# Performance work log

Hardware: AMD Instinct MI355X
Metric: run time of the kernel (lower is better)

The kernel has to match this reference:

```python
import jax, jax.numpy as jnp
import numpy as np

# Module hyperparameters (from init_kwargs)
N_S = 128                      # n_scalars
L2_IDX = (0, 1, 2, 3, 4, 5, 6) # l2_indices
N_L2 = len(L2_IDX) + 1         # selected l=2 kernels + their sum -> 8
H = 256                        # hidden multiplicity
B = 2048                       # batch
K = 8                          # number of kernels in kernel_t2s


def _w3j_222():
    """Real-basis Wigner 3j for (2e,2e)->2e, Frobenius norm 1 (e3nn convention).
    Built as tr(Qa Qb Qc) over an orthonormal basis of symmetric traceless 3x3
    matrices (the unique invariant 3-tensor on the 5-dim l=2 irrep)."""
    Q = np.zeros((5, 3, 3))
    s = 1.0 / np.sqrt(2.0)
    Q[0, 0, 1] = Q[0, 1, 0] = s
    Q[1, 1, 2] = Q[1, 2, 1] = s
    Q[2] = np.diag([-1.0, -1.0, 2.0]) / np.sqrt(6.0)
    Q[3, 0, 2] = Q[3, 2, 0] = s
    Q[4, 0, 0] = s
    Q[4, 1, 1] = -s
    C = np.einsum('aij,bjk,cki->abc', Q, Q, Q)
    return C / np.linalg.norm(C)

C222 = jnp.asarray(_w3j_222(), dtype=jnp.float32)

# e3nn FullyConnectedTensorProduct path normalization ('component'/'element'):
# coeff = sqrt((2*l_out+1) / sum over paths into same output of mul1*mul2)
C0 = float(np.sqrt(1.0 / (N_S**2 + N_L2**2)))            # paths into Hx0e: 0x0->0, 2x2->0
C2 = float(np.sqrt(5.0 / (2 * N_S * N_L2 + N_L2**2)))    # paths into Hx2e: 0x2, 2x0, 2x2
C2B = float(np.sqrt(5.0 / (3 * H**2)))                   # tp2 paths into 1x2e
INV_S5 = float(1.0 / np.sqrt(5.0))                       # w3j(l,l,0) = I/sqrt(2l+1), l=2


def setup_inputs() -> dict:
    key = jax.random.key(0)
    ks = jax.random.split(key, 10)
    f32 = jnp.float32
    return {
        'scalars': jax.random.normal(ks[0], (B, N_S), f32),
        'kernel_t2s': jax.random.normal(ks[1], (B, K, 5), f32),
        'W000': jax.random.normal(ks[2], (N_S, N_S, H), f32),
        'W220': jax.random.normal(ks[3], (N_L2, N_L2, H), f32),
        'W022': jax.random.normal(ks[4], (N_S, N_L2, H), f32),
        'W202': jax.random.normal(ks[5], (N_L2, N_S, H), f32),
        'W222': jax.random.normal(ks[6], (N_L2, N_L2, H), f32),
        'V022': jax.random.normal(ks[7], (H, H, 1), f32),
        'V202': jax.random.normal(ks[8], (H, H, 1), f32),
        'V222': jax.random.normal(ks[9], (H, H, 1), f32),
    }


def reference(scalars, kernel_t2s, W000, W220, W022, W202, W222, V022, V202, V222):
    ee = lambda *a: jnp.einsum(*a, optimize='optimal')
    idx = jnp.asarray(L2_IDX)
    # build tp input: [B, n_s] scalars  ++  [B, n_l2, 5] l=2 features
    t = jnp.concatenate([kernel_t2s[:, idx, :],
                         kernel_t2s.sum(axis=1, keepdims=True)], axis=1)  # [B, N_L2, 5]
    s = scalars                                                            # [B, N_S]

    # tp1(x, x): Hx0e + Hx2e
    y0 = C0 * (ee('uvw,zu,zv->zw', W000, s, s)
               + INV_S5 * ee('uvw,zui,zvi->zw', W220, t, t))               # [B, H]
    y2 = C2 * (INV_S5 * (ee('uvw,zu,zvk->zwk', W022, s, t)
                         + ee('uvw,zuk,zv->zwk', W202, t, s))
               + ee('uvw,ijk,zui,zvj->zwk', W222, C222, t, t))             # [B, H, 5]

    # tp2(y, y): 1x2e
    out = C2B * (INV_S5 * (ee('uvw,zu,zvk->zwk', V022, y0, y2)
                           + ee('uvw,zuk,zv->zwk', V202, y2, y0))
                 + ee('uvw,ijk,zui,zvj->zwk', V222, C222, y2, y2))         # [B, 1, 5]
    return out[:, 0, :]                                                    # [B, 5]
```

## Files before the change

kernel.cpp:

```cpp
#include <hip/hip_runtime.h>
#include <stdint.h>
#include <stddef.h>


#define NS     128
#define NL2    8
#define HH     256

#define KPAIR  8256
#define KPAD   8448
#define GLEN   64
#define KSPLIT 16
#define CHUNK  528
#define KT     16
#define NTILES 33

#define C0F  0.00779729f
#define C2F  0.04865619f
#define C2BF 0.005042948f
#define IS5  0.44721360f

constexpr size_t OFF_C222 = 0;
constexpr size_t OFF_PU   = 128;
constexpr size_t OFF_PV   = 8576;
constexpr size_t OFF_T    = 17024;
constexpr size_t OFF_GSYM = 98944;
constexpr size_t OFF_W1   = 230016;
constexpr size_t OFF_W222 = 754304;
constexpr size_t OFF_VBS  = 770688;
constexpr size_t OFF_VC   = 836224;
constexpr size_t OFF_Y0   = 901760;
constexpr size_t OFF_ACP  = 1426048;
constexpr size_t WS_FLOATS = 1950336;

#define SEG_T    81920
#define SEG_PUV  90368
#define SEG_W1   614656
#define SEG_W222 631040
#define SEG_VBS  696576
#define SEG_VC   762112
#define SEG_GS   893184
#define SEG_Y0   1417472

__global__ __launch_bounds__(256) void prep_k(
    const float* __restrict__ kt2s, const float* __restrict__ W022,
    const float* __restrict__ W202, const float* __restrict__ W222,
    const float* __restrict__ V022, const float* __restrict__ V202,
    const float* __restrict__ V222, float* __restrict__ ws) {
  const int tid = threadIdx.x;

  if (blockIdx.x == 0) {
    __shared__ float cv[125];
    __shared__ float inv;
    float val = 0.f;
    if (tid < 125) {
      float Q[45];
      #pragma unroll
      for (int q = 0; q < 45; ++q) Q[q] = 0.f;
      const float s2 = 0.70710678f, s6 = 0.40824829f;
      Q[0*9+0*3+1] = s2;  Q[0*9+1*3+0] = s2;
      Q[1*9+1*3+2] = s2;  Q[1*9+2*3+1] = s2;
      Q[2*9+0*3+0] = -s6; Q[2*9+1*3+1] = -s6; Q[2*9+2*3+2] = 2.f*s6;
      Q[3*9+0*3+2] = s2;  Q[3*9+2*3+0] = s2;
      Q[4*9+0*3+0] = s2;  Q[4*9+1*3+1] = -s2;
      const int a = tid/25, b = (tid/5)%5, c = tid%5;
      for (int i = 0; i < 3; ++i)
        for (int j = 0; j < 3; ++j)
          for (int k = 0; k < 3; ++k)
            val += Q[a*9+i*3+j]*Q[b*9+j*3+k]*Q[c*9+k*3+i];
      cv[tid] = val;
    }
    __syncthreads();
    if (tid == 0) {
      float sq = 0.f;
      for (int p = 0; p < 125; ++p) sq += cv[p]*cv[p];
      inv = 1.0f/sqrtf(sq);
    }
    __syncthreads();
    if (tid < 125) ws[OFF_C222 + tid] = val*inv;
    return;
  }

  int*   pu    = (int*)(ws + OFF_PU);
  int*   pv    = (int*)(ws + OFF_PV);
  const int stride = (gridDim.x - 1)*256;
  for (int i = (blockIdx.x - 1)*256 + tid; i < SEG_Y0; i += stride) {
    if (i < SEG_T) {
      int z = i/40, r = i - z*40, u = r/5, ii = r - u*5;
      float v;
      if (u < 7) v = kt2s[z*40 + u*5 + ii];
      else {
        v = 0.f;
        for (int k = 0; k < 8; ++k) v += kt2s[z*40 + k*5 + ii];
      }
      ws[OFF_T + i] = v;
    } else if (i < SEG_PUV) {
      int p = i - SEG_T;
      int u = 0, vv = 0;
      if (p < KPAIR) {
        int rem = p;
        while (rem >= NS - u) { rem -= NS - u; ++u; }
        vv = u + rem;
      } else if (p < KPAIR + 36) {
        int q = p - KPAIR;
        while (q >= NL2 - u) { q -= NL2 - u; ++u; }
        vv = u + q;
      }
      pu[p] = u; pv[p] = vv;
    } else if (i < SEG_W1) {
      int j = i - SEG_PUV;
      int u = j >> 12, col = j & 4095;
      float v;
      if (col < 2048) {
        int vv = col >> 8, w = col & 255;
        v = (C2F*IS5)*W022[(u*NL2 + vv)*HH + w];
      } else {
        int u2 = (col - 2048) >> 8, w = col & 255;
        v = (C2F*IS5)*W202[(u2*NS + u)*HH + w];
      }
      ws[OFF_W1 + j] = v;
    } else if (i < SEG_W222) {
      int j = i - SEG_W1;
      ws[OFF_W222 + j] = C2F*W222[j];
    } else if (i < SEG_VBS) {
      int j = i - SEG_W222;
      int u = j >> 8, c = j & 255;
      ws[OFF_VBS + j] = (C2BF*IS5)*(V022[u*HH + c] + V202[c*HH + u]);
    } else if (i < SEG_VC) {
      int j = i - SEG_VBS;
      ws[OFF_VC + j] = C2BF*V222[j];
    } else if (i < SEG_GS) {
      int j = i - SEG_VC;
      int z = j >> 6, q = j & 63;
      float v = 0.f;
      if (q < 36) {
        int qq = q, u = 0;
        while (qq >= NL2 - u) { qq -= NL2 - u; ++u; }
        int vv = u + qq;
        const float* kz = kt2s + (size_t)z*40;
        #pragma unroll
        for (int ii = 0; ii < 5; ++ii) {
          float tu, tv;
          if (u < 7) tu = kz[u*5 + ii];
          else { tu = 0.f; for (int k = 0; k < 8; ++k) tu += kz[k*5 + ii]; }
          if (vv < 7) tv = kz[vv*5 + ii];
          else { tv = 0.f; for (int k = 0; k < 8; ++k) tv += kz[k*5 + ii]; }
          v += tu*tv;
        }
      }
      ws[OFF_GSYM + j] = v;
    } else {
      ws[OFF_Y0 + (i - SEG_GS)] = 0.f;
    }
  }
}

__global__ __launch_bounds__(256) void gemm_y0_k(
    const float* __restrict__ s, const float* __restrict__ W000,
    const float* __restrict__ W220, float* __restrict__ ws) {
  const int* pu = (const int*)(ws + OFF_PU);
  const int* pv = (const int*)(ws + OFF_PV);
  const float* Gsym = ws + OFF_GSYM;
  float* y0 = ws + OFF_Y0;

  __shared__ float s_s[64][129];
  __shared__ __align__(16) float As[KT][64];
  __shared__ __align__(16) float Bs[KT][256];

  const int tid  = threadIdx.x;
  const int ks   = blockIdx.x & 15, mt = blockIdx.x >> 4;
  const int z0   = mt*64;
  const int kbase = ks*CHUNK;
  const int lane = tid & 63, wave = tid >> 6;
  const int tx   = tid & 31, ty   = tid >> 5;

  for (int e = 0; e < 8; ++e) {
    int f4 = e*256 + tid;
    int row = f4 >> 5, c4 = f4 & 31;
    float4 v = reinterpret_cast<const float4*>(s + (size_t)(z0 + row)*NS)[c4];
    s_s[row][c4*4+0] = v.x; s_s[row][c4*4+1] = v.y;
    s_s[row][c4*4+2] = v.z; s_s[row][c4*4+3] = v.w;
  }

  float acc[8][8];
  #pragma unroll
  for (int i = 0; i < 8; ++i)
    #pragma unroll
    for (int j = 0; j < 8; ++j) acc[i][j] = 0.f;

  for (int tt = 0; tt < NTILES; ++tt) {
    const int k0 = kbase + tt*KT;
    __syncthreads();
    #pragma unroll
    for (int e = 0; e < 4; ++e) {
      int row = e*4 + wave;
      int p = k0 + row;
      float4 val;
      if (p < KPAIR) {
        int u = pu[p], v = pv[p];
        float4 a = *reinterpret_cast<const float4*>(&W000[((size_t)(u*NS + v))*HH + lane*4]);
        if (u != v) {
          float4 b = *reinterpret_cast<const float4*>(&W000[((size_t)(v*NS + u))*HH + lane*4]);
          val = make_float4(C0F*(a.x+b.x), C0F*(a.y+b.y), C0F*(a.z+b.z), C0F*(a.w+b.w));
        } else {
          val = make_float4(C0F*a.x, C0F*a.y, C0F*a.z, C0F*a.w);
        }
      } else if (p < KPAIR + 36) {
        int u = pu[p], v = pv[p];
        const float sc = C0F*IS5;
        float4 a = *reinterpret_cast<const float4*>(&W220[(u*NL2 + v)*HH + lane*4]);
        if (u != v) {
          float4 b = *reinterpret_cast<const float4*>(&W220[(v*NL2 + u)*HH + lane*4]);
          val = make_float4(sc*(a.x+b.x), sc*(a.y+b.y), sc*(a.z+b.z), sc*(a.w+b.w));
        } else {
          val = make_float4(sc*a.x, sc*a.y, sc*a.z, sc*a.w);
        }
      } else {
        val = make_float4(0.f, 0.f, 0.f, 0.f);
      }
      *reinterpret_cast<float4*>(&Bs[row][lane*4]) = val;
    }
    #pragma unroll
    for (int e = 0; e < 4; ++e) {
      int kk = e*4 + wave;
      int k = k0 + kk;
      float a;
      if (k < KPAIR) a = s_s[lane][pu[k]]*s_s[lane][pv[k]];
      else {
        int q = k - KPAIR;
        a = (q < GLEN) ? Gsym[(size_t)(z0 + lane)*GLEN + q] : 0.f;
      }
      As[kk][lane] = a;
    }
    __syncthreads();
    #pragma unroll
    for (int kk = 0; kk < KT; ++kk) {
      float4 a0 = *reinterpret_cast<const float4*>(&As[kk][ty*8]);
      float4 a1 = *reinterpret_cast<const float4*>(&As[kk][ty*8+4]);
      float4 b0 = *reinterpret_cast<const float4*>(&Bs[kk][tx*4]);
      float4 b1 = *reinterpret_cast<const float4*>(&Bs[kk][128 + tx*4]);
      float am[8] = {a0.x,a0.y,a0.z,a0.w,a1.x,a1.y,a1.z,a1.w};
      float bn[8] = {b0.x,b0.y,b0.z,b0.w,b1.x,b1.y,b1.z,b1.w};
      #pragma unroll
      for (int mi = 0; mi < 8; ++mi)
        #pragma unroll
        for (int ni = 0; ni < 8; ++ni)
          acc[mi][ni] += am[mi]*bn[ni];
    }
  }
  #pragma unroll
  for (int mi = 0; mi < 8; ++mi) {
    int z = z0 + ty*8 + mi;
    #pragma unroll
    for (int ni = 0; ni < 8; ++ni) {
      int col = (ni < 4) ? (tx*4 + ni) : (128 + tx*4 + (ni-4));
      atomicAdd(&y0[(size_t)z*HH + col], acc[mi][ni]);
    }
  }
}

__global__ __launch_bounds__(256) void gemm_rm_k(
    const float* __restrict__ A, const float* __restrict__ B,
    float* __restrict__ C, int M, int N, int K) {
  __shared__ __align__(16) float As[32][68];
  __shared__ __align__(16) float Bs[32][68];
  const int tid = threadIdx.x, tx = tid & 15, ty = tid >> 4;
  const int n0 = blockIdx.x*64, m0 = blockIdx.y*64;
  float acc[4][4];
  #pragma unroll
  for (int i = 0; i < 4; ++i)
    #pragma unroll
    for (int j = 0; j < 4; ++j) acc[i][j] = 0.f;

  for (int k0 = 0; k0 < K; k0 += 32) {
    __syncthreads();
    #pragma unroll
    for (int e = 0; e < 2; ++e) {
      int r = e*32 + (tid >> 3);
      int kc = (tid & 7)*4;
      float4 v = *reinterpret_cast<const float4*>(&A[(size_t)(m0+r)*K + k0 + kc]);
      As[kc+0][r] = v.x; As[kc+1][r] = v.y; As[kc+2][r] = v.z; As[kc+3][r] = v.w;
    }
    #pragma unroll
    for (int e = 0; e < 2; ++e) {
      int idx = e*256 + tid;
      int r = idx >> 4, c4 = idx & 15;
      float4 v = *reinterpret_cast<const float4*>(&B[(size_t)(k0+r)*N + n0 + c4*4]);
      *reinterpret_cast<float4*>(&Bs[r][c4*4]) = v;
    }
    __syncthreads();
    #pragma unroll
    for (int kk = 0; kk < 32; ++kk) {
      float4 av = *reinterpret_cast<const float4*>(&As[kk][ty*4]);
      float4 bv = *reinterpret_cast<const float4*>(&Bs[kk][tx*4]);
      float am[4] = {av.x, av.y, av.z, av.w};
      float bn[4] = {bv.x, bv.y, bv.z, bv.w};
      #pragma unroll
      for (int i = 0; i < 4; ++i)
        #pragma unroll
        for (int j = 0; j < 4; ++j) acc[i][j] += am[i]*bn[j];
    }
  }
  #pragma unroll
  for (int i = 0; i < 4; ++i) {
    float4 v = make_float4(acc[i][0], acc[i][1], acc[i][2], acc[i][3]);
    *reinterpret_cast<float4*>(&C[(size_t)(m0 + ty*4 + i)*N + n0 + tx*4]) = v;
  }
}

__global__ __launch_bounds__(256) void mega_k(
    const float* __restrict__ scalars, const float* __restrict__ ws,
    float* __restrict__ out) {
  const float* tg    = ws + OFF_T;
  const float* W1    = ws + OFF_W1;
  const float* W222c = ws + OFF_W222;
  const float* VC    = ws + OFF_VC;
  const float* acp   = ws + OFF_ACP;
  const float* c222g = ws + OFF_C222;

  __shared__ float ts[8][40];
  __shared__ float c2s[125];
  __shared__ __align__(16) float sb[8][128];
  __shared__ __align__(16) float ovl[10240];
  float* tC  = ovl;
  float* RsF = ovl + 1600;
  float* y2s = ovl;

  const int tid = threadIdx.x;
  const int zg0 = blockIdx.x*8;
  const int lane = tid & 63, wv = tid >> 6;

  if (tid < 125) c2s[tid] = c222g[tid];
  for (int r = tid; r < 320; r += 256) {
    int z = r/40, c = r - z*40;
    ts[z][c] = tg[(size_t)(zg0 + z)*40 + c];
  }
  {
    int z = tid >> 5, c4 = tid & 31;
    float4 v = reinterpret_cast<const float4*>(scalars + (size_t)(zg0 + z)*NS)[c4];
    sb[z][c4*4+0] = v.x; sb[z][c4*4+1] = v.y;
    sb[z][c4*4+2] = v.z; sb[z][c4*4+3] = v.w;
  }
  __syncthreads();

  for (int idx = tid; idx < 1600; idx += 256) {
    int z = idx/200, r = idx - z*200, v = r/25, ik = r - v*25;
    int i = ik/5, k = ik - i*5;
    float a = 0.f;
    #pragma unroll
    for (int j = 0; j < 5; ++j) a += c2s[(i*5+j)*5 + k]*ts[z][v*5+j];
    tC[idx] = a;
  }
  __syncthreads();
  for (int idx = tid; idx < 2560; idx += 256) {
    int uv = idx/40, r = idx - uv*40, z = r/5, k = r - z*5;
    int u = uv >> 3, v = uv & 7;
    float a = 0.f;
    #pragma unroll
    for (int ii = 0; ii < 5; ++ii) a += ts[z][u*5+ii]*tC[z*200 + v*25 + ii*5 + k];
    RsF[idx] = a;
  }
  __syncthreads();

  float acc[8][5];
  #pragma unroll
  for (int z = 0; z < 8; ++z)
    #pragma unroll
    for (int k = 0; k < 5; ++k) acc[z][k] = 0.f;

  for (int vg = 0; vg < 4; ++vg) {
    float av[4][8];
    #pragma unroll
    for (int vi = 0; vi < 4; ++vi)
      #pragma unroll
      for (int z = 0; z < 8; ++z) av[vi][z] = 0.f;
    for (int u4 = 0; u4 < 128; u4 += 4) {
      float4 szv[8];
      #pragma unroll
      for (int z = 0; z < 8; ++z) szv[z] = *reinterpret_cast<const float4*>(&sb[z][u4]);
      #pragma unroll
      for (int uu = 0; uu < 4; ++uu) {
        #pragma unroll
        for (int vi = 0; vi < 4; ++vi) {
          float w1v = W1[(size_t)(u4+uu)*4096 + (vg*4+vi)*256 + tid];
          #pragma unroll
          for (int z = 0; z < 8; ++z) {
            float su = (uu==0)?szv[z].x:(uu==1)?szv[z].y:(uu==2)?szv[z].z:szv[z].w;
            av[vi][z] += su*w1v;
          }
        }
      }
    }
    #pragma unroll
    for (int vi = 0; vi < 4; ++vi) {
      int vmap = (vg*4 + vi) & 7;
      #pragma unroll
      for (int z = 0; z < 8; ++z)
        #pragma unroll
        for (int k = 0; k < 5; ++k)
          acc[z][k] += av[vi][z]*ts[z][vmap*5+k];
    }
  }

  for (int uv = 0; uv < 64; ++uv) {
    float wvv = W222c[uv*256 + tid];
    #pragma unroll
    for (int c4 = 0; c4 < 10; ++c4) {
      float4 rv = *reinterpret_cast<const float4*>(&RsF[uv*40 + c4*4]);
      acc[(c4*4+0)/5][(c4*4+0)%5] += wvv*rv.x;
      acc[(c4*4+1)/5][(c4*4+1)%5] += wvv*rv.y;
      acc[(c4*4+2)/5][(c4*4+2)%5] += wvv*rv.z;
      acc[(c4*4+3)/5][(c4*4+3)%5] += wvv*rv.w;
    }
  }

  __syncthreads();
  #pragma unroll
  for (int z = 0; z < 8; ++z)
    #pragma unroll
    for (int k = 0; k < 5; ++k)
      y2s[z*1280 + k*256 + tid] = acc[z][k];
  __syncthreads();

  float hacc[2][5][4];
  #pragma unroll
  for (int zz = 0; zz < 2; ++zz)
    #pragma unroll
    for (int i = 0; i < 5; ++i)
      #pragma unroll
      for (int j = 0; j < 4; ++j) hacc[zz][i][j] = 0.f;

  for (int u4 = 0; u4 < 256; u4 += 4) {
    float vc[4][4];
    #pragma unroll
    for (int uu = 0; uu < 4; ++uu)
      #pragma unroll
      for (int j = 0; j < 4; ++j)
        vc[uu][j] = VC[(size_t)(u4+uu)*256 + lane + 64*j];
    #pragma unroll
    for (int zz = 0; zz < 2; ++zz) {
      int z = wv*2 + zz;
      #pragma unroll
      for (int i = 0; i < 5; ++i) {
        float4 yv = *reinterpret_cast<const float4*>(&y2s[z*1280 + i*256 + u4]);
        float ya[4] = {yv.x, yv.y, yv.z, yv.w};
        #pragma unroll
        for (int uu = 0; uu < 4; ++uu)
          #pragma unroll
          for (int j = 0; j < 4; ++j)
            hacc[zz][i][j] += ya[uu]*vc[uu][j];
      }
    }
  }

  float outp[2][5];
  #pragma unroll
  for (int zz = 0; zz < 2; ++zz)
    #pragma unroll
    for (int k = 0; k < 5; ++k) outp[zz][k] = 0.f;

  for (int j = 0; j < 4; ++j) {
    int v = lane + 64*j;
    #pragma unroll
    for (int zz = 0; zz < 2; ++zz) {
      int z = wv*2 + zz;
      float y2v[5];
      #pragma unroll
      for (int jp = 0; jp < 5; ++jp) y2v[jp] = y2s[z*1280 + jp*256 + v];
      float avv = acp[(size_t)(zg0 + z)*256 + v];
      #pragma unroll
      for (int k = 0; k < 5; ++k) outp[zz][k] += avv*y2v[k];
      #pragma unroll
      for (int i = 0; i < 5; ++i) {
        float hv = hacc[zz][i][j];
        #pragma unroll
        for (int jp = 0; jp < 5; ++jp) {
          float pj = hv*y2v[jp];
          #pragma unroll
          for (int k = 0; k < 5; ++k)
            outp[zz][k] += pj*c2s[i*25 + jp*5 + k];
        }
      }
    }
  }

  #pragma unroll
  for (int zz = 0; zz < 2; ++zz)
    #pragma unroll
    for (int k = 0; k < 5; ++k) {
      float vsum = outp[zz][k];
      #pragma unroll
      for (int off = 32; off > 0; off >>= 1) vsum += __shfl_xor(vsum, off, 64);
      if (lane == 0) out[(size_t)(zg0 + wv*2 + zz)*5 + k] = vsum;
    }
}

extern "C" void kernel_launch(void* const* d_in, const int* in_sizes, int n_in,
                              void* d_out, int out_size, void* d_ws, size_t ws_size,
                              hipStream_t stream) {
  (void)in_sizes; (void)n_in; (void)out_size;
  const float* scalars = (const float*)d_in[0];
  const float* kt2s    = (const float*)d_in[1];
  const float* W000    = (const float*)d_in[2];
  const float* W220    = (const float*)d_in[3];
  const float* W022    = (const float*)d_in[4];
  const float* W202    = (const float*)d_in[5];
  const float* W222    = (const float*)d_in[6];
  const float* V022    = (const float*)d_in[7];
  const float* V202    = (const float*)d_in[8];
  const float* V222    = (const float*)d_in[9];
  float* out = (float*)d_out;
  float* ws  = (float*)d_ws;
  if (ws_size < WS_FLOATS*sizeof(float)) return;

  prep_k<<<1025, 256, 0, stream>>>(kt2s, W022, W202, W222, V022, V202, V222, ws);
  gemm_y0_k<<<512, 256, 0, stream>>>(scalars, W000, W220, ws);
  gemm_rm_k<<<dim3(4, 32), 256, 0, stream>>>(ws + OFF_Y0, ws + OFF_VBS,
                                             (float*)(ws + OFF_ACP), 2048, 256, 256);
  mega_k<<<256, 256, 0, stream>>>(scalars, ws, out);
}
```

Baseline: 585.0 us.

## Double-buffer y0 GEMM, split N tiles, transpose scalars, drop W1 repack

The y0 pair-GEMM now splits the 256 output columns into two 128-wide tiles, doubling the grid and halving accumulators per thread. It double-buffers the A/B shared tiles with register prefetch so the next tile's loads overlap the current tile's math. The A operand is read from column-major (transposed) copies of the scalars and the Gram matrix built in prep instead of a per-block shared scalar tile. The W022/W202 repack into W1 is removed, and mega_k reads the raw weights and applies the scale itself, which cuts prep work and workspace at the cost of strided weight loads and redundant B-tile loads across the two N halves.

```diff
diff --git a/kernel.cpp b/kernel.cpp
--- a/kernel.cpp
+++ b/kernel.cpp
@@ -6,6 +6,7 @@
 #define NS     128
 #define NL2    8
 #define HH     256
+#define NB     2048
 
 #define KPAIR  8256
 #define KPAD   8448
@@ -24,27 +25,27 @@
 constexpr size_t OFF_PU   = 128;
 constexpr size_t OFF_PV   = 8576;
 constexpr size_t OFF_T    = 17024;
-constexpr size_t OFF_GSYM = 98944;
-constexpr size_t OFF_W1   = 230016;
-constexpr size_t OFF_W222 = 754304;
-constexpr size_t OFF_VBS  = 770688;
-constexpr size_t OFF_VC   = 836224;
-constexpr size_t OFF_Y0   = 901760;
-constexpr size_t OFF_ACP  = 1426048;
-constexpr size_t WS_FLOATS = 1950336;
+constexpr size_t OFF_W222 = 98944;
+constexpr size_t OFF_VBS  = 115328;
+constexpr size_t OFF_VC   = 180864;
+constexpr size_t OFF_ST   = 246400;
+constexpr size_t OFF_GT   = 508544;
+constexpr size_t OFF_Y0   = 639616;
+constexpr size_t OFF_ACP  = 1163904;
+constexpr size_t WS_FLOATS = 1688192;
 
 #define SEG_T    81920
 #define SEG_PUV  90368
-#define SEG_W1   614656
-#define SEG_W222 631040
-#define SEG_VBS  696576
-#define SEG_VC   762112
-#define SEG_GS   893184
-#define SEG_Y0   1417472
+#define SEG_W222 106752
+#define SEG_VBS  172288
+#define SEG_VC   237824
+#define SEG_ST   499968
+#define SEG_GT   631040
+#define SEG_END  1155328
 
 __global__ __launch_bounds__(256) void prep_k(
-    const float* __restrict__ kt2s, const float* __restrict__ W022,
-    const float* __restrict__ W202, const float* __restrict__ W222,
+    const float* __restrict__ scalars, const float* __restrict__ kt2s,
+    const float* __restrict__ W222,
     const float* __restrict__ V022, const float* __restrict__ V202,
     const float* __restrict__ V222, float* __restrict__ ws) {
   const int tid = threadIdx.x;
@@ -81,10 +82,10 @@
     return;
   }
 
-  int*   pu    = (int*)(ws + OFF_PU);
-  int*   pv    = (int*)(ws + OFF_PV);
+  int* pu = (int*)(ws + OFF_PU);
+  int* pv = (int*)(ws + OFF_PV);
   const int stride = (gridDim.x - 1)*256;
-  for (int i = (blockIdx.x - 1)*256 + tid; i < SEG_Y0; i += stride) {
+  for (int i = (blockIdx.x - 1)*256 + tid; i < SEG_END; i += stride) {
     if (i < SEG_T) {
       int z = i/40, r = i - z*40, u = r/5, ii = r - u*5;
       float v;
@@ -107,20 +108,8 @@
         vv = u + q;
       }
       pu[p] = u; pv[p] = vv;
-    } else if (i < SEG_W1) {
+    } else if (i < SEG_W222) {
       int j = i - SEG_PUV;
-      int u = j >> 12, col = j & 4095;
-      float v;
-      if (col < 2048) {
-        int vv = col >> 8, w = col & 255;
-        v = (C2F*IS5)*W022[(u*NL2 + vv)*HH + w];
-      } else {
-        int u2 = (col - 2048) >> 8, w = col & 255;
-        v = (C2F*IS5)*W202[(u2*NS + u)*HH + w];
-      }
-      ws[OFF_W1 + j] = v;
-    } else if (i < SEG_W222) {
-      int j = i - SEG_W1;
       ws[OFF_W222 + j] = C2F*W222[j];
     } else if (i < SEG_VBS) {
       int j = i - SEG_W222;
@@ -129,9 +118,13 @@
     } else if (i < SEG_VC) {
       int j = i - SEG_VBS;
       ws[OFF_VC + j] = C2BF*V222[j];
-    } else if (i < SEG_GS) {
+    } else if (i < SEG_ST) {
       int j = i - SEG_VC;
-      int z = j >> 6, q = j & 63;
+      int u = j >> 11, z = j & 2047;
+      ws[OFF_ST + j] = scalars[(size_t)z*NS + u];
+    } else if (i < SEG_GT) {
+      int j = i - SEG_ST;
+      int q = j >> 11, z = j & 2047;
       float v = 0.f;
       if (q < 36) {
         int qq = q, u = 0;
@@ -148,114 +141,135 @@
           v += tu*tv;
         }
       }
-      ws[OFF_GSYM + j] = v;
+      ws[OFF_GT + j] = v;
     } else {
-      ws[OFF_Y0 + (i - SEG_GS)] = 0.f;
+      ws[OFF_Y0 + (i - SEG_GT)] = 0.f;
     }
   }
 }
 
-__global__ __launch_bounds__(256) void gemm_y0_k(
-    const float* __restrict__ s, const float* __restrict__ W000,
-    const float* __restrict__ W220, float* __restrict__ ws) {
+__global__ __launch_bounds__(256, 4) void gemm_y0_k(
+    const float* __restrict__ W000, const float* __restrict__ W220,
+    float* __restrict__ ws) {
   const int* pu = (const int*)(ws + OFF_PU);
   const int* pv = (const int*)(ws + OFF_PV);
-  const float* Gsym = ws + OFF_GSYM;
+  const float* sT = ws + OFF_ST;
+  const float* gT = ws + OFF_GT;
   float* y0 = ws + OFF_Y0;
 
-  __shared__ float s_s[64][129];
-  __shared__ __align__(16) float As[KT][64];
-  __shared__ __align__(16) float Bs[KT][256];
-
-  const int tid  = threadIdx.x;
-  const int ks   = blockIdx.x & 15, mt = blockIdx.x >> 4;
-  const int z0   = mt*64;
+  __shared__ __align__(16) float As[2][KT][64];
+  __shared__ __align__(16) float Bs[2][KT][128];
+
+  const int tid = threadIdx.x;
+  const int bid = blockIdx.x;
+  const int ks = bid & 15, mtnt = bid >> 4;
+  const int mt = mtnt >> 1, nt = mtnt & 1;
+  const int z0 = mt*64, n0 = nt*128;
   const int kbase = ks*CHUNK;
-  const int lane = tid & 63, wave = tid >> 6;
-  const int tx   = tid & 31, ty   = tid >> 5;
-
-  for (int e = 0; e < 8; ++e) {
-    int f4 = e*256 + tid;
-    int row = f4 >> 5, c4 = f4 & 31;
-    float4 v = reinterpret_cast<const float4*>(s + (size_t)(z0 + row)*NS)[c4];
-    s_s[row][c4*4+0] = v.x; s_s[row][c4*4+1] = v.y;
-    s_s[row][c4*4+2] = v.z; s_s[row][c4*4+3] = v.w;
-  }
-
-  float acc[8][8];
-  #pragma unroll
-  for (int i = 0; i < 8; ++i)
-    #pragma unroll
-    for (int j = 0; j < 8; ++j) acc[i][j] = 0.f;
-
-  for (int tt = 0; tt < NTILES; ++tt) {
-    const int k0 = kbase + tt*KT;
-    __syncthreads();
-    #pragma unroll
-    for (int e = 0; e < 4; ++e) {
-      int row = e*4 + wave;
-      int p = k0 + row;
+  const int m = tid & 63, w = tid >> 6;
+  const int tx = tid & 31, ty = tid >> 5;
+
+  float4 bReg[2];
+  float  aReg[4];
+
+  auto load_tile = [&](int t) {
+    const int k0 = kbase + t*KT;
+    #pragma unroll
+    for (int e = 0; e < 2; ++e) {
+      int idx = e*256 + tid;
+      int r = idx >> 5, col = (idx & 31)*4;
+      int p = k0 + r;
       float4 val;
       if (p < KPAIR) {
         int u = pu[p], v = pv[p];
-        float4 a = *reinterpret_cast<const float4*>(&W000[((size_t)(u*NS + v))*HH + lane*4]);
+        float4 a = *reinterpret_cast<const float4*>(
+            &W000[((size_t)u*NS + v)*HH + n0 + col]);
         if (u != v) {
-          float4 b = *reinterpret_cast<const float4*>(&W000[((size_t)(v*NS + u))*HH + lane*4]);
-          val = make_float4(C0F*(a.x+b.x), C0F*(a.y+b.y), C0F*(a.z+b.z), C0F*(a.w+b.w));
+          float4 b = *reinterpret_cast<const float4*>(
+              &W000[((size_t)v*NS + u)*HH + n0 + col]);
+          val = make_float4(C0F*(a.x+b.x), C0F*(a.y+b.y),
+                            C0F*(a.z+b.z), C0F*(a.w+b.w));
         } else {
           val = make_float4(C0F*a.x, C0F*a.y, C0F*a.z, C0F*a.w);
         }
       } else if (p < KPAIR + 36) {
         int u = pu[p], v = pv[p];
         const float sc = C0F*IS5;
-        float4 a = *reinterpret_cast<const float4*>(&W220[(u*NL2 + v)*HH + lane*4]);
+        float4 a = *reinterpret_cast<const float4*>(
+            &W220[(u*NL2 + v)*HH + n0 + col]);
         if (u != v) {
-          float4 b = *reinterpret_cast<const float4*>(&W220[(v*NL2 + u)*HH + lane*4]);
-          val = make_float4(sc*(a.x+b.x), sc*(a.y+b.y), sc*(a.z+b.z), sc*(a.w+b.w));
+          float4 b = *reinterpret_cast<const float4*>(
+              &W220[(v*NL2 + u)*HH + n0 + col]);
+          val = make_float4(sc*(a.x+b.x), sc*(a.y+b.y),
+                            sc*(a.z+b.z), sc*(a.w+b.w));
         } else {
           val = make_float4(sc*a.x, sc*a.y, sc*a.z, sc*a.w);
         }
       } else {
         val = make_float4(0.f, 0.f, 0.f, 0.f);
       }
-      *reinterpret_cast<float4*>(&Bs[row][lane*4]) = val;
+      bReg[e] = val;
     }
     #pragma unroll
     for (int e = 0; e < 4; ++e) {
-      int kk = e*4 + wave;
-      int k = k0 + kk;
+      int k = k0 + e*4 + w;
       float a;
-      if (k < KPAIR) a = s_s[lane][pu[k]]*s_s[lane][pv[k]];
-      else {
+      if (k < KPAIR) {
+        a = sT[(size_t)pu[k]*NB + z0 + m] * sT[(size_t)pv[k]*NB + z0 + m];
+      } else {
         int q = k - KPAIR;
-        a = (q < GLEN) ? Gsym[(size_t)(z0 + lane)*GLEN + q] : 0.f;
-      }
-      As[kk][lane] = a;
-    }
+        a = (q < GLEN) ? gT[(size_t)q*NB + z0 + m] : 0.f;
+      }
+      aReg[e] = a;
+    }
+  };
+  auto store_tile = [&](int buf) {
+    #pragma unroll
+    for (int e = 0; e < 2; ++e) {
+      int idx = e*256 + tid;
+      int r = idx >> 5, col = (idx & 31)*4;
+      *reinterpret_cast<float4*>(&Bs[buf][r][col]) = bReg[e];
+    }
+    #pragma unroll
+    for (int e = 0; e < 4; ++e) As[buf][e*4 + w][m] = aReg[e];
+  };
+
+  float acc[8][4];
+  #pragma unroll
+  for (int i = 0; i < 8; ++i)
+    #pragma unroll
+    for (int j = 0; j < 4; ++j) acc[i][j] = 0.f;
+
+  load_tile(0);
+  store_tile(0);
+  __syncthreads();
+
+  for (int t = 0; t < NTILES; ++t) {
+    if (t + 1 < NTILES) load_tile(t + 1);
+    const int cur = t & 1;
+    #pragma unroll
+    for (int kk = 0; kk < KT; ++kk) {
+      float4 a0 = *reinterpret_cast<const float4*>(&As[cur][kk][ty*8]);
+      float4 a1 = *reinterpret_cast<const float4*>(&As[cur][kk][ty*8+4]);
+      float4 bv = *reinterpret_cast<const float4*>(&Bs[cur][kk][tx*4]);
+      float am[8] = {a0.x,a0.y,a0.z,a0.w,a1.x,a1.y,a1.z,a1.w};
+      float bn[4] = {bv.x,bv.y,bv.z,bv.w};
+      #pragma unroll
+      for (int mi = 0; mi < 8; ++mi)
+        #pragma unroll
+        for (int ni = 0; ni < 4; ++ni)
+          acc[mi][ni] += am[mi]*bn[ni];
+    }
+    if (t + 1 < NTILES) store_tile(cur ^ 1);
     __syncthreads();
-    #pragma unroll
-    for (int kk = 0; kk < KT; ++kk) {
-      float4 a0 = *reinterpret_cast<const float4*>(&As[kk][ty*8]);
-      float4 a1 = *reinterpret_cast<const float4*>(&As[kk][ty*8+4]);
-      float4 b0 = *reinterpret_cast<const float4*>(&Bs[kk][tx*4]);
-      float4 b1 = *reinterpret_cast<const float4*>(&Bs[kk][128 + tx*4]);
-      float am[8] = {a0.x,a0.y,a0.z,a0.w,a1.x,a1.y,a1.z,a1.w};
-      float bn[8] = {b0.x,b0.y,b0.z,b0.w,b1.x,b1.y,b1.z,b1.w};
-      #pragma unroll
-      for (int mi = 0; mi < 8; ++mi)
-        #pragma unroll
-        for (int ni = 0; ni < 8; ++ni)
-          acc[mi][ni] += am[mi]*bn[ni];
-    }
-  }
+  }
+
   #pragma unroll
   for (int mi = 0; mi < 8; ++mi) {
     int z = z0 + ty*8 + mi;
     #pragma unroll
-    for (int ni = 0; ni < 8; ++ni) {
-      int col = (ni < 4) ? (tx*4 + ni) : (128 + tx*4 + (ni-4));
-      atomicAdd(&y0[(size_t)z*HH + col], acc[mi][ni]);
-    }
+    for (int ni = 0; ni < 4; ++ni)
+      atomicAdd(&y0[(size_t)z*HH + n0 + tx*4 + ni], acc[mi][ni]);
   }
 }
 
@@ -309,10 +323,10 @@
 }
 
 __global__ __launch_bounds__(256) void mega_k(
-    const float* __restrict__ scalars, const float* __restrict__ ws,
+    const float* __restrict__ scalars, const float* __restrict__ W022,
+    const float* __restrict__ W202, const float* __restrict__ ws,
     float* __restrict__ out) {
   const float* tg    = ws + OFF_T;
-  const float* W1    = ws + OFF_W1;
   const float* W222c = ws + OFF_W222;
   const float* VC    = ws + OFF_VC;
   const float* acp   = ws + OFF_ACP;
@@ -380,9 +394,12 @@
       for (int z = 0; z < 8; ++z) szv[z] = *reinterpret_cast<const float4*>(&sb[z][u4]);
       #pragma unroll
       for (int uu = 0; uu < 4; ++uu) {
+        int u = u4 + uu;
         #pragma unroll
         for (int vi = 0; vi < 4; ++vi) {
-          float w1v = W1[(size_t)(u4+uu)*4096 + (vg*4+vi)*256 + tid];
+          float w1v = (vg < 2)
+            ? W022[((size_t)u*NL2 + (vg*4+vi))*HH + tid]
+            : W202[((size_t)((vg-2)*4+vi)*NS + u)*HH + tid];
           #pragma unroll
           for (int z = 0; z < 8; ++z) {
             float su = (uu==0)?szv[z].x:(uu==1)?szv[z].y:(uu==2)?szv[z].z:szv[z].w;
@@ -395,10 +412,12 @@
     for (int vi = 0; vi < 4; ++vi) {
       int vmap = (vg*4 + vi) & 7;
       #pragma unroll
-      for (int z = 0; z < 8; ++z)
+      for (int z = 0; z < 8; ++z) {
+        float avs = (C2F*IS5)*av[vi][z];
         #pragma unroll
         for (int k = 0; k < 5; ++k)
-          acc[z][k] += av[vi][z]*ts[z][vmap*5+k];
+          acc[z][k] += avs*ts[z][vmap*5+k];
+      }
     }
   }
 
@@ -513,9 +532,9 @@
   float* ws  = (float*)d_ws;
   if (ws_size < WS_FLOATS*sizeof(float)) return;
 
-  prep_k<<<1025, 256, 0, stream>>>(kt2s, W022, W202, W222, V022, V202, V222, ws);
-  gemm_y0_k<<<512, 256, 0, stream>>>(scalars, W000, W220, ws);
+  prep_k<<<1025, 256, 0, stream>>>(scalars, kt2s, W222, V022, V202, V222, ws);
+  gemm_y0_k<<<1024, 256, 0, stream>>>(W000, W220, ws);
   gemm_rm_k<<<dim3(4, 32), 256, 0, stream>>>(ws + OFF_Y0, ws + OFF_VBS,
                                              (float*)(ws + OFF_ACP), 2048, 256, 256);
-  mega_k<<<256, 256, 0, stream>>>(scalars, ws, out);
+  mega_k<<<256, 256, 0, stream>>>(scalars, W022, W202, ws, out);
 }
```

Result: faster. 498.1 us (-14.8%).
